# Kernel tuning notes

Hardware: AMD Instinct MI355X
Metric: run time of the kernel (lower is better)

## Reference

```python
import jax, jax.numpy as jnp
import numpy as np

Q_DIM = 256; KV_DIM = 256; C = 32; N_HEAD = 8; OUT_DIM = 256
B1, B2, LQ, LK = 1, 128, 256, 256


def _glorot(key, shape, gain=1.0):
    fan_in, fan_out = shape[-2], shape[-1]
    std = gain * np.sqrt(2.0 / float(fan_in + fan_out))
    dev = np.sqrt(3.0) * std
    return jax.random.uniform(key, shape, jnp.float32, -dev, dev)


def setup_inputs() -> dict:
    key = jax.random.key(0)
    ks = jax.random.split(key, 12)
    q_data = jax.random.normal(ks[0], (B1, B2, LQ, Q_DIM), jnp.float32)
    kv_data = jax.random.normal(ks[1], (B1, B2, LK, KV_DIM), jnp.float32)
    bias = jax.random.normal(ks[2], (B1, B2, N_HEAD, LQ, LK), jnp.float32)
    nonbatched_bias = jax.random.normal(ks[3], (B1, N_HEAD, LQ, LK), jnp.float32)
    # torch Linear weights are [out, in]; original init is zeros but we use
    # glorot for a non-degenerate numerical baseline.
    Wq = _glorot(ks[4], (N_HEAD * C, Q_DIM))
    Wk = _glorot(ks[5], (N_HEAD * C, KV_DIM))
    Wv = _glorot(ks[6], (N_HEAD * C, KV_DIM))
    Wg = _glorot(ks[7], (N_HEAD * C, Q_DIM))
    bg = jnp.ones((N_HEAD * C,), jnp.float32)  # bias_init=1.0
    Wo = _glorot(ks[8], (OUT_DIM, N_HEAD * C))
    bo = jnp.zeros((OUT_DIM,), jnp.float32)
    return dict(q_data=q_data, kv_data=kv_data, bias=bias,
                nonbatched_bias=nonbatched_bias, Wq=Wq, Wk=Wk, Wv=Wv,
                Wg=Wg, bg=bg, Wo=Wo, bo=bo)


def reference(q_data, kv_data, bias, nonbatched_bias, Wq, Wk, Wv, Wg, bg, Wo, bo):
    c = C
    # projections: [b1,b2,len,n_head,c]
    q = (q_data @ Wq.T).reshape(*q_data.shape[:-1], N_HEAD, c) * (c ** -0.5)
    k = (kv_data @ Wk.T).reshape(*kv_data.shape[:-1], N_HEAD, c)
    v = (kv_data @ Wv.T).reshape(*kv_data.shape[:-1], N_HEAD, c)
    # logits: [b1,b2,n_head,len_q,len_kv]
    logits = jnp.einsum('bsqhc,bskhc->bshqk', q, k)
    logits = logits + bias + nonbatched_bias[:, None]
    weights = jax.nn.softmax(logits, axis=-1)
    weighted_avg = jnp.einsum('bshqk,bskhc->bsqhc', weights, v)
    gate = jax.nn.sigmoid((q_data @ Wg.T + bg).reshape(*q_data.shape[:-1], N_HEAD, c))
    weighted_avg = weighted_avg * gate
    out = weighted_avg.reshape(*weighted_avg.shape[:-2], N_HEAD * c) @ Wo.T + bo
    return out
```

## Files before the change

kernel.cpp:

```cpp
#include <hip/hip_runtime.h>
#include <hip/hip_bf16.h>

#define NB2 128
#define LQK 256
#define DIM 256
#define NH 8
#define CC 32

typedef __bf16 bf16x8 __attribute__((ext_vector_type(8)));
typedef __bf16 bf16x4 __attribute__((ext_vector_type(4)));
typedef float f32x4 __attribute__((ext_vector_type(4)));

#define MFMA16 __builtin_amdgcn_mfma_f32_16x16x32_bf16

#define TP 72

#define NTOK ((size_t)NB2 * LQK * NH * CC)

static __device__ __forceinline__ void gload_lds16(const void* g, void* l) {
    __builtin_amdgcn_global_load_lds(
        (const __attribute__((address_space(1))) unsigned int*)g,
        (__attribute__((address_space(3))) unsigned int*)l,
        16, 0, 0);
}

__global__ __launch_bounds__(256) void k_wcvt(
    const float* __restrict__ Wq, const float* __restrict__ Wk,
    const float* __restrict__ Wv, const float* __restrict__ Wg,
    const float* __restrict__ Wo, __bf16* __restrict__ dst)
{
    int i = (blockIdx.x * 256 + threadIdx.x) * 4;
    int mat = i >> 16;
    int off = i & 65535;
    const float* src = (mat == 0) ? Wq : (mat == 1) ? Wk : (mat == 2) ? Wv
                      : (mat == 3) ? Wg : Wo;
    f32x4 v = *(const f32x4*)(src + off);
    __bf16* d = dst + ((size_t)mat << 16) + off;
    d[0] = (__bf16)v[0]; d[1] = (__bf16)v[1]; d[2] = (__bf16)v[2]; d[3] = (__bf16)v[3];
}

__global__ __launch_bounds__(256) void k_acvt(
    const float* __restrict__ qd, const float* __restrict__ kvd,
    __bf16* __restrict__ qbf, __bf16* __restrict__ kvbf)
{
    size_t i = ((size_t)blockIdx.x * 256 + threadIdx.x) * 8;
    const float* src;
    __bf16* dst;
    if (i < NTOK) { src = qd + i; dst = qbf + i; }
    else          { src = kvd + (i - NTOK); dst = kvbf + (i - NTOK); }
    f32x4 a = *(const f32x4*)src;
    f32x4 b = *(const f32x4*)(src + 4);
    bf16x8 r;
    r[0] = (__bf16)a[0]; r[1] = (__bf16)a[1]; r[2] = (__bf16)a[2]; r[3] = (__bf16)a[3];
    r[4] = (__bf16)b[0]; r[5] = (__bf16)b[1]; r[6] = (__bf16)b[2]; r[7] = (__bf16)b[3];
    *(bf16x8*)dst = r;
}

__global__ __launch_bounds__(256, 2) void k_proj(
    const __bf16* __restrict__ qbf, const __bf16* __restrict__ kvbf,
    const __bf16* __restrict__ wBF, const float* __restrict__ bg,
    __bf16* __restrict__ wsq, __bf16* __restrict__ wsk,
    __bf16* __restrict__ wsvT, __bf16* __restrict__ wsgT)
{
    __shared__ __bf16 At[2][128][TP];
    __shared__ __bf16 Bt[2][128][TP];

    const int mb = blockIdx.x, nb = blockIdx.y;
    const int t = nb >> 1;
    const __bf16* X = (t == 0 || t == 3) ? qbf : kvbf;
    const __bf16* W = wBF + ((size_t)t << 16) + (size_t)((nb & 1) * 128) * 256;

    const int tid = threadIdx.x;
    const int lane = tid & 63, w = tid >> 6;
    const int g = lane >> 4, kg = g * 8, c0 = lane & 15;
    const int mq = (w >> 1) * 64, nq = (w & 1) * 64;
    const int m0 = mb * 128;
    const int srow = tid >> 1, shalf = (tid & 1) * 32;

    f32x4 acc[4][4] = {};
    bf16x8 av[4], bv[4];
    auto load_stage = [&](int kit) {
        const __bf16* ap = X + (size_t)(m0 + srow) * DIM + kit * 64 + shalf;
        const __bf16* bp = W + (size_t)srow * 256 + kit * 64 + shalf;
#pragma unroll
        for (int j = 0; j < 4; j++) {
            av[j] = *(const bf16x8*)(ap + j * 8);
            bv[j] = *(const bf16x8*)(bp + j * 8);
        }
    };
    auto write_stage = [&](int buf) {
#pragma unroll
        for (int j = 0; j < 4; j++) {
            *(bf16x8*)(&At[buf][srow][shalf + j * 8]) = av[j];
            *(bf16x8*)(&Bt[buf][srow][shalf + j * 8]) = bv[j];
        }
    };

    load_stage(0);
    write_stage(0);
    __syncthreads();

#pragma unroll
    for (int kit = 0; kit < 4; kit++) {
        if (kit < 3) load_stage(kit + 1);
        const int cur = kit & 1;
#pragma unroll
        for (int ks = 0; ks < 2; ks++) {
            bf16x8 af[4], bf_[4];
#pragma unroll
            for (int mi = 0; mi < 4; mi++)
                af[mi] = *(const bf16x8*)(&At[cur][mq + mi * 16 + c0][ks * 32 + kg]);
#pragma unroll
            for (int ni = 0; ni < 4; ni++)
                bf_[ni] = *(const bf16x8*)(&Bt[cur][nq + ni * 16 + c0][ks * 32 + kg]);
#pragma unroll
            for (int mi = 0; mi < 4; mi++)
#pragma unroll
                for (int ni = 0; ni < 4; ni++)
                    acc[mi][ni] = MFMA16(af[mi], bf_[ni], acc[mi][ni], 0, 0, 0);
        }
        if (kit < 3) write_stage(cur ^ 1);
        __syncthreads();
    }

#pragma unroll
    for (int ni = 0; ni < 4; ni++) {
        const int nloc = (nb & 1) * 128 + nq + ni * 16 + c0;
        const int h = nloc >> 5, c = nloc & 31;
        const float bg_ = (t == 3) ? bg[nloc] : 0.0f;
#pragma unroll
        for (int mi = 0; mi < 4; mi++) {
            const int mbase = m0 + mq + mi * 16 + g * 4;
            const int b2 = mbase >> 8;
            if (t == 2) {
                bf16x4 pk;
#pragma unroll
                for (int reg = 0; reg < 4; reg++) pk[reg] = (__bf16)acc[mi][ni][reg];
                *(bf16x4*)(&wsvT[((size_t)(b2 * NH + h) * CC + c) * LQK + (mbase & 255)]) = pk;
            } else if (t == 3) {
                bf16x4 pk;
#pragma unroll
                for (int reg = 0; reg < 4; reg++)
                    pk[reg] = (__bf16)(1.0f / (1.0f + __expf(-(acc[mi][ni][reg] + bg_))));
                *(bf16x4*)(&wsgT[((size_t)(b2 * NH + h) * CC + c) * LQK + (mbase & 255)]) = pk;
            } else {
#pragma unroll
                for (int reg = 0; reg < 4; reg++) {
                    const int l = (mbase + reg) & 255;
                    float v = acc[mi][ni][reg];
                    size_t idx = ((size_t)(b2 * NH + h) * LQK + l) * CC + c;
                    if (t == 0) wsq[idx] = (__bf16)(v * 0.17677669529663689f);
                    else        wsk[idx] = (__bf16)v;
                }
            }
        }
    }
}

__global__ __launch_bounds__(256, 3) void k_attn(
    const __bf16* __restrict__ wsq, const __bf16* __restrict__ wsk,
    const __bf16* __restrict__ wsvT, const __bf16* __restrict__ wsgT,
    const float* __restrict__ bias, const float* __restrict__ nbb,
    __bf16* __restrict__ wswa)
{
    __shared__ float Bl[2][64][64];
    __shared__ __bf16 P[4][16][TP];

    const int tid = threadIdx.x;
    const int bid = blockIdx.x;
    const int b2 = bid >> 5, h = (bid >> 2) & 7, qt = bid & 3;
    const int lane = tid & 63, w = tid >> 6;
    const int g = lane >> 4, kg = g * 8, c0 = lane & 15;
    const int qbase = qt * 64 + w * 16;
    const int q = qbase + c0;
    const int rw = w * 16 + c0;

    const __bf16* qp = wsq + (size_t)(b2 * NH + h) * LQK * CC;
    const __bf16* kp = wsk + (size_t)(b2 * NH + h) * LQK * CC;
    const __bf16* vT = wsvT + (size_t)(b2 * NH + h) * CC * LQK;
    const __bf16* gT = wsgT + (size_t)(b2 * NH + h) * CC * LQK;
    const float* np = nbb + ((size_t)h * LQK + q) * LQK;
    const float* bblk = bias + ((size_t)(b2 * NH + h) * LQK + qt * 64) * LQK;

    auto stage = [&](int buf, int c) {
        const int rbase = tid >> 4;
        const int jj = tid & 15;
#pragma unroll
        for (int i = 0; i < 4; i++) {
            const int row = i * 16 + rbase;
            const int u = jj ^ (row & 7);
            const float* src = bblk + (size_t)row * LQK + c * 64 + u * 4;
            gload_lds16(src, &Bl[buf][i * 16 + w * 4][0]);
        }
    };

    bf16x8 qf = *(const bf16x8*)(qp + (size_t)q * CC + kg);

    stage(0, 0);
    __syncthreads();

    float l = 0.0f;
    f32x4 o[2] = {};

#pragma unroll
    for (int c = 0; c < 4; c++) {
        const int cur = c & 1;
        if (c < 3) stage(cur ^ 1, c + 1);

        float csum = 0.0f;
#pragma unroll
        for (int j = 0; j < 4; j++) {
            const int su = ((j * 4 + g) ^ (rw & 7)) * 4;
            f32x4 b4 = *(const f32x4*)(&Bl[cur][rw][su]);
            f32x4 n4 = *(const f32x4*)(np + c * 64 + j * 16 + g * 4);
            bf16x8 kf = *(const bf16x8*)(kp + (size_t)((c * 4 + j) * 16 + c0) * CC + kg);
            f32x4 cc;
#pragma unroll
            for (int r2 = 0; r2 < 4; r2++) cc[r2] = b4[r2] + n4[r2];
            f32x4 s = MFMA16(kf, qf, cc, 0, 0, 0);
            bf16x4 pk;
#pragma unroll
            for (int r2 = 0; r2 < 4; r2++) {
                float e = __expf(s[r2]);
                csum += e;
                pk[r2] = (__bf16)e;
            }
            *(bf16x4*)(&P[w][c0][j * 16 + g * 4]) = pk;
        }
        l += csum;
#pragma unroll
        for (int kt2 = 0; kt2 < 2; kt2++) {
            bf16x8 pa = *(const bf16x8*)(&P[w][c0][kt2 * 32 + kg]);
#pragma unroll
            for (int vn = 0; vn < 2; vn++) {
                bf16x8 vb = *(const bf16x8*)(vT + (size_t)(vn * 16 + c0) * LQK + c * 64 + kt2 * 32 + kg);
                o[vn] = MFMA16(pa, vb, o[vn], 0, 0, 0);
            }
        }
        if (c < 3) __syncthreads();
    }

    l += __shfl_xor(l, 16);
    l += __shfl_xor(l, 32);
    const float inv = 1.0f / l;

#pragma unroll
    for (int vn = 0; vn < 2; vn++) {
        const int c = vn * 16 + c0;
        bf16x4 g4 = *(const bf16x4*)(gT + (size_t)c * LQK + qbase + g * 4);
#pragma unroll
        for (int reg = 0; reg < 4; reg++) {
            const int row = qbase + g * 4 + reg;
            const float invr = __shfl(inv, g * 4 + reg, 64);
            const float val = o[vn][reg] * invr * (float)g4[reg];
            wswa[((size_t)(b2 * LQK + row)) * (NH * CC) + h * CC + c] = (__bf16)val;
        }
    }
}

__global__ __launch_bounds__(256, 2) void k_out(
    const __bf16* __restrict__ wa, const __bf16* __restrict__ wBF,
    const float* __restrict__ bo, float* __restrict__ out)
{
    __shared__ __bf16 At[2][128][TP];
    __shared__ __bf16 Bt[2][128][TP];

    const int mb = blockIdx.x, nb = blockIdx.y;
    const __bf16* W = wBF + ((size_t)4 << 16) + (size_t)(nb * 128) * 256;

    const int tid = threadIdx.x;
    const int lane = tid & 63, w = tid >> 6;
    const int g = lane >> 4, kg = g * 8, c0 = lane & 15;
    const int mq = (w >> 1) * 64, nq = (w & 1) * 64;
    const int m0 = mb * 128;
    const int srow = tid >> 1, shalf = (tid & 1) * 32;

    f32x4 acc[4][4] = {};
    bf16x8 av[4], bv[4];
    auto load_stage = [&](int kit) {
        const __bf16* ap = wa + (size_t)(m0 + srow) * 256 + kit * 64 + shalf;
        const __bf16* bp = W + (size_t)srow * 256 + kit * 64 + shalf;
#pragma unroll
        for (int j = 0; j < 4; j++) {
            av[j] = *(const bf16x8*)(ap + j * 8);
            bv[j] = *(const bf16x8*)(bp + j * 8);
        }
    };
    auto write_stage = [&](int buf) {
#pragma unroll
        for (int j = 0; j < 4; j++) {
            *(bf16x8*)(&At[buf][srow][shalf + j * 8]) = av[j];
            *(bf16x8*)(&Bt[buf][srow][shalf + j * 8]) = bv[j];
        }
    };

    load_stage(0);
    write_stage(0);
    __syncthreads();

#pragma unroll
    for (int kit = 0; kit < 4; kit++) {
        if (kit < 3) load_stage(kit + 1);
        const int cur = kit & 1;
#pragma unroll
        for (int ks = 0; ks < 2; ks++) {
            bf16x8 af[4], bf_[4];
#pragma unroll
            for (int mi = 0; mi < 4; mi++)
                af[mi] = *(const bf16x8*)(&At[cur][mq + mi * 16 + c0][ks * 32 + kg]);
#pragma unroll
            for (int ni = 0; ni < 4; ni++)
                bf_[ni] = *(const bf16x8*)(&Bt[cur][nq + ni * 16 + c0][ks * 32 + kg]);
#pragma unroll
            for (int mi = 0; mi < 4; mi++)
#pragma unroll
                for (int ni = 0; ni < 4; ni++)
                    acc[mi][ni] = MFMA16(af[mi], bf_[ni], acc[mi][ni], 0, 0, 0);
        }
        if (kit < 3) write_stage(cur ^ 1);
        __syncthreads();
    }

#pragma unroll
    for (int ni = 0; ni < 4; ni++) {
        const int n = nb * 128 + nq + ni * 16 + c0;
        const float bo_ = bo[n];
#pragma unroll
        for (int mi = 0; mi < 4; mi++) {
            const int mbase = m0 + mq + mi * 16 + g * 4;
#pragma unroll
            for (int reg = 0; reg < 4; reg++)
                out[(size_t)(mbase + reg) * 256 + n] = acc[mi][ni][reg] + bo_;
        }
    }
}

extern "C" void kernel_launch(void* const* d_in, const int* in_sizes, int n_in,
                              void* d_out, int out_size, void* d_ws, size_t ws_size,
                              hipStream_t stream) {
    const float* qd  = (const float*)d_in[0];
    const float* kvd = (const float*)d_in[1];
    const float* bias = (const float*)d_in[2];
    const float* nbb = (const float*)d_in[3];
    const float* Wq = (const float*)d_in[4];
    const float* Wk = (const float*)d_in[5];
    const float* Wv = (const float*)d_in[6];
    const float* Wg = (const float*)d_in[7];
    const float* bg = (const float*)d_in[8];
    const float* Wo = (const float*)d_in[9];
    const float* bo = (const float*)d_in[10];
    float* out = (float*)d_out;

    __bf16* ws = (__bf16*)d_ws;
    __bf16* wsq  = ws;
    __bf16* wsk  = wsq + NTOK;
    __bf16* wsvT = wsk + NTOK;
    __bf16* wsgT = wsvT + NTOK;
    __bf16* wBF  = wsgT + NTOK;
    __bf16* qbf  = wBF + 5 * 65536;
    __bf16* kvbf = qbf + NTOK;
    __bf16* wswa = qbf;

    k_wcvt<<<dim3(320), 256, 0, stream>>>(Wq, Wk, Wv, Wg, Wo, wBF);
    k_acvt<<<dim3(8192), 256, 0, stream>>>(qd, kvd, qbf, kvbf);
    k_proj<<<dim3(256, 8), 256, 0, stream>>>(qbf, kvbf, wBF, bg,
                                             wsq, wsk, wsvT, wsgT);
    k_attn<<<dim3(4096), 256, 0, stream>>>(wsq, wsk, wsvT, wsgT, bias, nbb, wswa);
    k_out<<<dim3(256, 2), 256, 0, stream>>>(wswa, wBF, bo, out);
}
```

Measured before the change: 186.0 us.

## Stage K and V tiles through LDS and remap blocks across XCDs

K and V chunks are now loaded asynchronously into double-buffered, swizzled LDS tiles alongside the bias tile, instead of being read directly from global memory inside the MFMA loop. Block indices are remapped so the four q-tiles of one head run on the same XCD, which should improve L2 reuse of K, V and bias. Launch bounds drop from 3 to 2 blocks per SIMD to cover the extra LDS and registers, which may reduce occupancy.

```diff
diff --git a/kernel.cpp b/kernel.cpp
--- a/kernel.cpp
+++ b/kernel.cpp
@@ -157,18 +157,24 @@
     }
 }
 
-__global__ __launch_bounds__(256, 3) void k_attn(
+__global__ __launch_bounds__(256, 2) void k_attn(
     const __bf16* __restrict__ wsq, const __bf16* __restrict__ wsk,
     const __bf16* __restrict__ wsvT, const __bf16* __restrict__ wsgT,
     const float* __restrict__ bias, const float* __restrict__ nbb,
     __bf16* __restrict__ wswa)
 {
-    __shared__ float Bl[2][64][64];
+    __shared__ float  Bl[2][64][64];
+    __shared__ __bf16 Kl[2][2048];
+    __shared__ __bf16 Vl[2][2048];
     __shared__ __bf16 P[4][16][TP];
 
     const int tid = threadIdx.x;
-    const int bid = blockIdx.x;
-    const int b2 = bid >> 5, h = (bid >> 2) & 7, qt = bid & 3;
+    const int u0 = blockIdx.x;
+    const int xcd = u0 & 7, slot = u0 >> 3;
+    const int head = xcd + 8 * (slot >> 2);
+    const int qt = slot & 3;
+    const int b2 = head >> 3, h = head & 7;
+
     const int lane = tid & 63, w = tid >> 6;
     const int g = lane >> 4, kg = g * 8, c0 = lane & 15;
     const int qbase = qt * 64 + w * 16;
@@ -183,14 +189,23 @@
     const float* bblk = bias + ((size_t)(b2 * NH + h) * LQK + qt * 64) * LQK;
 
     auto stage = [&](int buf, int c) {
-        const int rbase = tid >> 4;
-        const int jj = tid & 15;
+        const int rbase = tid >> 4, jj = tid & 15;
 #pragma unroll
         for (int i = 0; i < 4; i++) {
             const int row = i * 16 + rbase;
-            const int u = jj ^ (row & 7);
-            const float* src = bblk + (size_t)row * LQK + c * 64 + u * 4;
-            gload_lds16(src, &Bl[buf][i * 16 + w * 4][0]);
+            const int uu = jj ^ (row & 7);
+            gload_lds16(bblk + (size_t)row * LQK + c * 64 + uu * 4,
+                        &Bl[buf][i * 16 + w * 4][0]);
+        }
+        {
+            const int su = (lane & 3) ^ ((lane >> 3) & 3);
+            gload_lds16(kp + (size_t)(c * 64 + w * 16 + (lane >> 2)) * CC + su * 8,
+                        &Kl[buf][w * 512]);
+        }
+        {
+            const int su = (lane & 7) ^ (lane >> 3);
+            gload_lds16(vT + (size_t)(w * 8 + (lane >> 3)) * LQK + c * 64 + su * 8,
+                        &Vl[buf][w * 512]);
         }
     };
 
@@ -213,7 +228,8 @@
             const int su = ((j * 4 + g) ^ (rw & 7)) * 4;
             f32x4 b4 = *(const f32x4*)(&Bl[cur][rw][su]);
             f32x4 n4 = *(const f32x4*)(np + c * 64 + j * 16 + g * 4);
-            bf16x8 kf = *(const bf16x8*)(kp + (size_t)((c * 4 + j) * 16 + c0) * CC + kg);
+            bf16x8 kf = *(const bf16x8*)(
+                &Kl[cur][((j * 16 + c0) * 4 + (g ^ ((c0 >> 1) & 3))) * 8]);
             f32x4 cc;
 #pragma unroll
             for (int r2 = 0; r2 < 4; r2++) cc[r2] = b4[r2] + n4[r2];
@@ -233,7 +249,8 @@
             bf16x8 pa = *(const bf16x8*)(&P[w][c0][kt2 * 32 + kg]);
 #pragma unroll
             for (int vn = 0; vn < 2; vn++) {
-                bf16x8 vb = *(const bf16x8*)(vT + (size_t)(vn * 16 + c0) * LQK + c * 64 + kt2 * 32 + kg);
+                bf16x8 vb = *(const bf16x8*)(
+                    &Vl[cur][((vn * 16 + c0) * 8 + ((kt2 * 4 + g) ^ (c0 & 7))) * 8]);
                 o[vn] = MFMA16(pa, vb, o[vn], 0, 0, 0);
             }
         }
```

New measurement: 165.5 us. 11.0% less time.

## Pipeline attention with per-wave bias staging, register prefetch and XCD-aware block mapping

Applied to the files above, without the earlier changes.

The attention kernel now stages the bias tile per wave into its own double-buffered LDS region, two chunks ahead, which removes the block-wide __syncthreads. K, V and the non-batched bias fragments are prefetched into double-buffered registers one chunk ahead. Explicit vmcnt waits with sched barriers order the loads against compute. Block indices are remapped so that the four query tiles of a head land on the same XCD for L2 reuse. The cost is higher register pressure and fragile hand-counted waitcnt values that must match the number of loads issued.

```diff
diff --git a/kernel.cpp b/kernel.cpp
--- a/kernel.cpp
+++ b/kernel.cpp
@@ -23,6 +23,9 @@
         (__attribute__((address_space(3))) unsigned int*)l,
         16, 0, 0);
 }
+
+#define WAITV(N) do { asm volatile("s_waitcnt vmcnt(" #N ")" ::: "memory"); \
+                      __builtin_amdgcn_sched_barrier(0); } while (0)
 
 __global__ __launch_bounds__(256) void k_wcvt(
     const float* __restrict__ Wq, const float* __restrict__ Wk,
@@ -163,41 +166,62 @@
     const float* __restrict__ bias, const float* __restrict__ nbb,
     __bf16* __restrict__ wswa)
 {
-    __shared__ float Bl[2][64][64];
-    __shared__ __bf16 P[4][16][TP];
+    __shared__ float  Bw[4][2][16][64];
+    __shared__ __bf16 P[4][16][66];
 
     const int tid = threadIdx.x;
-    const int bid = blockIdx.x;
-    const int b2 = bid >> 5, h = (bid >> 2) & 7, qt = bid & 3;
+    const int u0 = blockIdx.x;
+    const int xcd = u0 & 7, slot = u0 >> 3;
+    const int head = xcd + 8 * (slot >> 2);
+    const int qt = slot & 3;
+    const int b2 = head >> 3, h = head & 7;
+
     const int lane = tid & 63, w = tid >> 6;
     const int g = lane >> 4, kg = g * 8, c0 = lane & 15;
     const int qbase = qt * 64 + w * 16;
     const int q = qbase + c0;
-    const int rw = w * 16 + c0;
 
     const __bf16* qp = wsq + (size_t)(b2 * NH + h) * LQK * CC;
     const __bf16* kp = wsk + (size_t)(b2 * NH + h) * LQK * CC;
     const __bf16* vT = wsvT + (size_t)(b2 * NH + h) * CC * LQK;
     const __bf16* gT = wsgT + (size_t)(b2 * NH + h) * CC * LQK;
     const float* np = nbb + ((size_t)h * LQK + q) * LQK;
-    const float* bblk = bias + ((size_t)(b2 * NH + h) * LQK + qt * 64) * LQK;
-
-    auto stage = [&](int buf, int c) {
-        const int rbase = tid >> 4;
-        const int jj = tid & 15;
+    const float* bpw = bias + ((size_t)(b2 * NH + h) * LQK + qbase) * LQK;
+
+    auto stageB = [&](int buf, int c) {
+        const int rsub = lane >> 4, jj = lane & 15;
 #pragma unroll
         for (int i = 0; i < 4; i++) {
-            const int row = i * 16 + rbase;
-            const int u = jj ^ (row & 7);
-            const float* src = bblk + (size_t)row * LQK + c * 64 + u * 4;
-            gload_lds16(src, &Bl[buf][i * 16 + w * 4][0]);
+            const int row = i * 4 + rsub;
+            const int uu = jj ^ row;
+            gload_lds16(bpw + (size_t)row * LQK + c * 64 + uu * 4,
+                        &Bw[w][buf][i * 4][0]);
         }
     };
 
     bf16x8 qf = *(const bf16x8*)(qp + (size_t)q * CC + kg);
 
-    stage(0, 0);
-    __syncthreads();
+    bf16x8 kfb[2][4], vfb[2][4];
+    f32x4 nbr[2][4];
+    auto loadKVN = [&](int buf, int c) {
+#pragma unroll
+        for (int j = 0; j < 4; j++)
+            kfb[buf][j] = *(const bf16x8*)(kp + (size_t)(c * 64 + j * 16 + c0) * CC + kg);
+#pragma unroll
+        for (int h2 = 0; h2 < 2; h2++)
+#pragma unroll
+            for (int vn = 0; vn < 2; vn++)
+                vfb[buf][h2 * 2 + vn] = *(const bf16x8*)(
+                    vT + (size_t)(vn * 16 + c0) * LQK + c * 64 + h2 * 32 + kg);
+#pragma unroll
+        for (int j = 0; j < 4; j++)
+            nbr[buf][j] = *(const f32x4*)(np + c * 64 + j * 16 + g * 4);
+    };
+
+    stageB(0, 0);
+    loadKVN(0, 0);
+    stageB(1, 1);
+    WAITV(4);
 
     float l = 0.0f;
     f32x4 o[2] = {};
@@ -205,19 +229,17 @@
 #pragma unroll
     for (int c = 0; c < 4; c++) {
         const int cur = c & 1;
-        if (c < 3) stage(cur ^ 1, c + 1);
+        if (c < 3) loadKVN(cur ^ 1, c + 1);
 
         float csum = 0.0f;
 #pragma unroll
         for (int j = 0; j < 4; j++) {
-            const int su = ((j * 4 + g) ^ (rw & 7)) * 4;
-            f32x4 b4 = *(const f32x4*)(&Bl[cur][rw][su]);
-            f32x4 n4 = *(const f32x4*)(np + c * 64 + j * 16 + g * 4);
-            bf16x8 kf = *(const bf16x8*)(kp + (size_t)((c * 4 + j) * 16 + c0) * CC + kg);
+            const int phys = (j * 4 + g) ^ c0;
+            f32x4 b4 = *(const f32x4*)(&Bw[w][cur][c0][phys * 4]);
             f32x4 cc;
 #pragma unroll
-            for (int r2 = 0; r2 < 4; r2++) cc[r2] = b4[r2] + n4[r2];
-            f32x4 s = MFMA16(kf, qf, cc, 0, 0, 0);
+            for (int r2 = 0; r2 < 4; r2++) cc[r2] = b4[r2] + nbr[cur][j][r2];
+            f32x4 s = MFMA16(kfb[cur][j], qf, cc, 0, 0, 0);
             bf16x4 pk;
 #pragma unroll
             for (int r2 = 0; r2 < 4; r2++) {
@@ -228,16 +250,19 @@
             *(bf16x4*)(&P[w][c0][j * 16 + g * 4]) = pk;
         }
         l += csum;
-#pragma unroll
-        for (int kt2 = 0; kt2 < 2; kt2++) {
-            bf16x8 pa = *(const bf16x8*)(&P[w][c0][kt2 * 32 + kg]);
-#pragma unroll
-            for (int vn = 0; vn < 2; vn++) {
-                bf16x8 vb = *(const bf16x8*)(vT + (size_t)(vn * 16 + c0) * LQK + c * 64 + kt2 * 32 + kg);
-                o[vn] = MFMA16(pa, vb, o[vn], 0, 0, 0);
-            }
-        }
-        if (c < 3) __syncthreads();
+
+        if (c < 2) stageB(cur, c + 2);
+
+#pragma unroll
+        for (int h2 = 0; h2 < 2; h2++) {
+            bf16x8 pa = *(const bf16x8*)(&P[w][c0][h2 * 32 + kg]);
+#pragma unroll
+            for (int vn = 0; vn < 2; vn++)
+                o[vn] = MFMA16(pa, vfb[cur][h2 * 2 + vn], o[vn], 0, 0, 0);
+        }
+
+        if (c < 2)      WAITV(4);
+        else if (c == 2) WAITV(0);
     }
 
     l += __shfl_xor(l, 16);
```

Measured after the change: 183.1 us. No clear change (-1.6%).
